# Kernel tuning notes

Hardware: AMD Instinct MI355X
Metric: run time of the kernel (lower is better)

## Reference

```python
import jax, jax.numpy as jnp
import numpy as np

E = 1024
H = 16
D = E // H
B = 32
S = 1024


def _layernorm(x, gamma, beta, eps=1e-5):
    mu = jnp.mean(x, axis=-1, keepdims=True)
    var = jnp.var(x, axis=-1, keepdims=True)
    return (x - mu) * jax.lax.rsqrt(var + eps) * gamma + beta


def setup_inputs() -> dict:
    key = jax.random.key(0)
    ks = jax.random.split(key, 16)
    w = lambda k, shape: jax.random.normal(k, shape, dtype=jnp.float32) * 0.02
    return {
        "img_feat": jax.random.normal(ks[0], (B, S, E), dtype=jnp.float32),
        "heat_feat": jax.random.normal(ks[1], (B, E), dtype=jnp.float32),
        "W_img": w(ks[2], (E, E)), "b_img": jnp.zeros((E,), jnp.float32),
        "W_heat": w(ks[3], (E, E)), "b_heat": jnp.zeros((E,), jnp.float32),
        "Wq": w(ks[4], (E, E)), "bq": jnp.zeros((E,), jnp.float32),
        "Wk": w(ks[5], (E, E)), "bk": jnp.zeros((E,), jnp.float32),
        "Wv": w(ks[6], (E, E)), "bv": jnp.zeros((E,), jnp.float32),
        "Wo": w(ks[7], (E, E)), "bo": jnp.zeros((E,), jnp.float32),
        "gamma": jnp.ones((E,), jnp.float32),
        "beta": jnp.zeros((E,), jnp.float32),
    }


def reference(img_feat, heat_feat, W_img, b_img, W_heat, b_heat,
              Wq, bq, Wk, bk, Wv, bv, Wo, bo, gamma, beta):
    # projections (torch Linear: x @ W.T + b)
    proj_heat = (heat_feat @ W_heat.T + b_heat)[:, None, :]        # [B,1,E]
    proj_img = img_feat @ W_img.T + b_img                          # [B,S,E]
    # multi-head attention, KV seq len = 1
    q = (proj_img @ Wq.T + bq).reshape(B, S, H, D)
    k = (proj_heat @ Wk.T + bk).reshape(B, 1, H, D)
    v = (proj_heat @ Wv.T + bv).reshape(B, 1, H, D)
    scale = 1.0 / np.sqrt(D).astype(np.float32)
    scores = jnp.einsum('bshd,bthd->bhst', q, k) * scale           # [B,H,S,1]
    attn = jax.nn.softmax(scores, axis=-1)                         # == ones
    ctx = jnp.einsum('bhst,bthd->bshd', attn, v).reshape(B, S, E)
    attn_out = ctx @ Wo.T + bo                                     # [B,S,E]
    # residual + LayerNorm (dropout is identity in eval)
    return _layernorm(img_feat + attn_out, gamma, beta)
```

## Files before the change

kernel.cpp:

```cpp
#include <hip/hip_runtime.h>


#define E_DIM 1024
#define B_DIM 32
#define S_DIM 1024

__global__ __launch_bounds__(256) void gemv_f32(
        const float* __restrict__ W,
        const float* __restrict__ bias,
        const float* __restrict__ x,
        float* __restrict__ y) {
    int wave = threadIdx.x >> 6;
    int lane = threadIdx.x & 63;
    int out_idx = (blockIdx.x << 2) + wave;
    int b = out_idx >> 10;
    int e = out_idx & (E_DIM - 1);
    const float4* w4 = reinterpret_cast<const float4*>(W + (size_t)e * E_DIM);
    const float4* x4 = reinterpret_cast<const float4*>(x + (size_t)b * E_DIM);
    float acc = 0.f;
    #pragma unroll
    for (int p = 0; p < 4; ++p) {
        float4 wv = w4[p * 64 + lane];
        float4 xv = x4[p * 64 + lane];
        acc += wv.x * xv.x + wv.y * xv.y + wv.z * xv.z + wv.w * xv.w;
    }
    #pragma unroll
    for (int off = 32; off; off >>= 1)
        acc += __shfl_down(acc, off, 64);
    if (lane == 0) y[out_idx] = acc + bias[e];
}

__global__ __launch_bounds__(256) void resid_layernorm(
        const float* __restrict__ img,
        const float* __restrict__ a,
        const float* __restrict__ gamma,
        const float* __restrict__ beta,
        float* __restrict__ out) {
    const int row = blockIdx.x;
    const int b = row >> 10;
    const int t = threadIdx.x;

    const float4* imgp = reinterpret_cast<const float4*>(img + (size_t)row * E_DIM);
    const float4* ap   = reinterpret_cast<const float4*>(a + (size_t)b * E_DIM);

    float4 iv = imgp[t];
    float4 av = ap[t];

    float x0 = iv.x + av.x;
    float x1 = iv.y + av.y;
    float x2 = iv.z + av.z;
    float x3 = iv.w + av.w;

    float s = x0 + x1 + x2 + x3;
    float q = x0 * x0 + x1 * x1 + x2 * x2 + x3 * x3;

    #pragma unroll
    for (int off = 32; off; off >>= 1) {
        s += __shfl_down(s, off, 64);
        q += __shfl_down(q, off, 64);
    }

    __shared__ float ssum[4], sqq[4];
    int wv = t >> 6, ln = t & 63;
    if (ln == 0) { ssum[wv] = s; sqq[wv] = q; }
    __syncthreads();
    if (t == 0) {
        float S = ssum[0] + ssum[1] + ssum[2] + ssum[3];
        float Q = sqq[0] + sqq[1] + sqq[2] + sqq[3];
        float mu = S * (1.0f / E_DIM);
        float var = Q * (1.0f / E_DIM) - mu * mu;
        ssum[0] = mu;
        sqq[0] = rsqrtf(var + 1e-5f);
    }
    __syncthreads();
    float mu = ssum[0];
    float rstd = sqq[0];

    const float4* gp = reinterpret_cast<const float4*>(gamma) + t;
    const float4* bp = reinterpret_cast<const float4*>(beta) + t;
    float4 gv = *gp, bv = *bp;

    float4 ov;
    ov.x = (x0 - mu) * rstd * gv.x + bv.x;
    ov.y = (x1 - mu) * rstd * gv.y + bv.y;
    ov.z = (x2 - mu) * rstd * gv.z + bv.z;
    ov.w = (x3 - mu) * rstd * gv.w + bv.w;

    reinterpret_cast<float4*>(out + (size_t)row * E_DIM)[t] = ov;
}

extern "C" void kernel_launch(void* const* d_in, const int* in_sizes, int n_in,
                              void* d_out, int out_size, void* d_ws, size_t ws_size,
                              hipStream_t stream) {
    const float* heat   = (const float*)d_in[1];
    const float* W_heat = (const float*)d_in[4];
    const float* b_heat = (const float*)d_in[5];
    const float* Wv     = (const float*)d_in[10];
    const float* bvv    = (const float*)d_in[11];
    const float* Wo     = (const float*)d_in[12];
    const float* bo     = (const float*)d_in[13];
    const float* img    = (const float*)d_in[0];
    const float* gamma  = (const float*)d_in[14];
    const float* beta   = (const float*)d_in[15];
    float* out = (float*)d_out;

    float* ws = (float*)d_ws;
    float* tt = ws;
    float* vv = ws + B_DIM * E_DIM;
    float* aa = ws + 2 * B_DIM * E_DIM;

    const int n_be = B_DIM * E_DIM;
    const int gemv_blocks = n_be / 4;

    gemv_f32<<<gemv_blocks, 256, 0, stream>>>(W_heat, b_heat, heat, tt);
    gemv_f32<<<gemv_blocks, 256, 0, stream>>>(Wv, bvv, tt, vv);
    gemv_f32<<<gemv_blocks, 256, 0, stream>>>(Wo, bo, vv, aa);

    resid_layernorm<<<B_DIM * S_DIM, 256, 0, stream>>>(img, aa, gamma, beta, out);
}
```

Before: 295.1 us.

## Reuse weight rows across 8 batches in GEMV and use wave-per-row layernorm

```diff
diff --git a/kernel.cpp b/kernel.cpp
--- a/kernel.cpp
+++ b/kernel.cpp
@@ -5,29 +5,40 @@
 #define B_DIM 32
 #define S_DIM 1024
 
-__global__ __launch_bounds__(256) void gemv_f32(
+__global__ __launch_bounds__(256) void gemv8_f32(
         const float* __restrict__ W,
         const float* __restrict__ bias,
         const float* __restrict__ x,
         float* __restrict__ y) {
-    int wave = threadIdx.x >> 6;
-    int lane = threadIdx.x & 63;
-    int out_idx = (blockIdx.x << 2) + wave;
-    int b = out_idx >> 10;
-    int e = out_idx & (E_DIM - 1);
+    const int w    = blockIdx.x * 4 + (threadIdx.x >> 6);
+    const int lane = threadIdx.x & 63;
+    const int e    = w >> 2;
+    const int b0   = (w & 3) * 8;
+
     const float4* w4 = reinterpret_cast<const float4*>(W + (size_t)e * E_DIM);
-    const float4* x4 = reinterpret_cast<const float4*>(x + (size_t)b * E_DIM);
-    float acc = 0.f;
+    float acc[8] = {0.f, 0.f, 0.f, 0.f, 0.f, 0.f, 0.f, 0.f};
+
     #pragma unroll
     for (int p = 0; p < 4; ++p) {
         float4 wv = w4[p * 64 + lane];
-        float4 xv = x4[p * 64 + lane];
-        acc += wv.x * xv.x + wv.y * xv.y + wv.z * xv.z + wv.w * xv.w;
+        #pragma unroll
+        for (int j = 0; j < 8; ++j) {
+            const float4* x4 =
+                reinterpret_cast<const float4*>(x + (size_t)(b0 + j) * E_DIM);
+            float4 xv = x4[p * 64 + lane];
+            acc[j] += wv.x * xv.x + wv.y * xv.y + wv.z * xv.z + wv.w * xv.w;
+        }
     }
+
+    const float be = bias[e];
     #pragma unroll
-    for (int off = 32; off; off >>= 1)
-        acc += __shfl_down(acc, off, 64);
-    if (lane == 0) y[out_idx] = acc + bias[e];
+    for (int j = 0; j < 8; ++j) {
+        float v = acc[j];
+        #pragma unroll
+        for (int off = 32; off; off >>= 1)
+            v += __shfl_down(v, off, 64);
+        if (lane == 0) y[(size_t)(b0 + j) * E_DIM + e] = v + be;
+    }
 }
 
 __global__ __launch_bounds__(256) void resid_layernorm(
@@ -36,62 +47,59 @@
         const float* __restrict__ gamma,
         const float* __restrict__ beta,
         float* __restrict__ out) {
-    const int row = blockIdx.x;
-    const int b = row >> 10;
-    const int t = threadIdx.x;
+    const int row  = blockIdx.x * 4 + (threadIdx.x >> 6);
+    const int lane = threadIdx.x & 63;
+    const int b    = row >> 10;
 
-    const float4* imgp = reinterpret_cast<const float4*>(img + (size_t)row * E_DIM);
-    const float4* ap   = reinterpret_cast<const float4*>(a + (size_t)b * E_DIM);
+    const float4* ip = reinterpret_cast<const float4*>(img + (size_t)row * E_DIM);
+    const float4* ap = reinterpret_cast<const float4*>(a + (size_t)b * E_DIM);
 
-    float4 iv = imgp[t];
-    float4 av = ap[t];
-
-    float x0 = iv.x + av.x;
-    float x1 = iv.y + av.y;
-    float x2 = iv.z + av.z;
-    float x3 = iv.w + av.w;
-
-    float s = x0 + x1 + x2 + x3;
-    float q = x0 * x0 + x1 * x1 + x2 * x2 + x3 * x3;
+    float4 xv[4];
+    float s = 0.f, q = 0.f;
+    #pragma unroll
+    for (int p = 0; p < 4; ++p) {
+        float4 iv = ip[p * 64 + lane];
+        float4 av = ap[p * 64 + lane];
+        float4 x;
+        x.x = iv.x + av.x;
+        x.y = iv.y + av.y;
+        x.z = iv.z + av.z;
+        x.w = iv.w + av.w;
+        xv[p] = x;
+        s += x.x + x.y + x.z + x.w;
+        q += x.x * x.x + x.y * x.y + x.z * x.z + x.w * x.w;
+    }
 
     #pragma unroll
     for (int off = 32; off; off >>= 1) {
-        s += __shfl_down(s, off, 64);
-        q += __shfl_down(q, off, 64);
+        s += __shfl_xor(s, off, 64);
+        q += __shfl_xor(q, off, 64);
     }
 
-    __shared__ float ssum[4], sqq[4];
-    int wv = t >> 6, ln = t & 63;
-    if (ln == 0) { ssum[wv] = s; sqq[wv] = q; }
-    __syncthreads();
-    if (t == 0) {
-        float S = ssum[0] + ssum[1] + ssum[2] + ssum[3];
-        float Q = sqq[0] + sqq[1] + sqq[2] + sqq[3];
-        float mu = S * (1.0f / E_DIM);
-        float var = Q * (1.0f / E_DIM) - mu * mu;
-        ssum[0] = mu;
-        sqq[0] = rsqrtf(var + 1e-5f);
+    const float mu   = s * (1.0f / E_DIM);
+    const float rstd = rsqrtf(q * (1.0f / E_DIM) - mu * mu + 1e-5f);
+
+    const float4* gp = reinterpret_cast<const float4*>(gamma);
+    const float4* bp = reinterpret_cast<const float4*>(beta);
+    float4* op = reinterpret_cast<float4*>(out + (size_t)row * E_DIM);
+
+    #pragma unroll
+    for (int p = 0; p < 4; ++p) {
+        float4 g  = gp[p * 64 + lane];
+        float4 be = bp[p * 64 + lane];
+        float4 o;
+        o.x = (xv[p].x - mu) * rstd * g.x + be.x;
+        o.y = (xv[p].y - mu) * rstd * g.y + be.y;
+        o.z = (xv[p].z - mu) * rstd * g.z + be.z;
+        o.w = (xv[p].w - mu) * rstd * g.w + be.w;
+        op[p * 64 + lane] = o;
     }
-    __syncthreads();
-    float mu = ssum[0];
-    float rstd = sqq[0];
-
-    const float4* gp = reinterpret_cast<const float4*>(gamma) + t;
-    const float4* bp = reinterpret_cast<const float4*>(beta) + t;
-    float4 gv = *gp, bv = *bp;
-
-    float4 ov;
-    ov.x = (x0 - mu) * rstd * gv.x + bv.x;
-    ov.y = (x1 - mu) * rstd * gv.y + bv.y;
-    ov.z = (x2 - mu) * rstd * gv.z + bv.z;
-    ov.w = (x3 - mu) * rstd * gv.w + bv.w;
-
-    reinterpret_cast<float4*>(out + (size_t)row * E_DIM)[t] = ov;
 }
 
 extern "C" void kernel_launch(void* const* d_in, const int* in_sizes, int n_in,
                               void* d_out, int out_size, void* d_ws, size_t ws_size,
                               hipStream_t stream) {
+    const float* img    = (const float*)d_in[0];
     const float* heat   = (const float*)d_in[1];
     const float* W_heat = (const float*)d_in[4];
     const float* b_heat = (const float*)d_in[5];
@@ -99,7 +107,6 @@
     const float* bvv    = (const float*)d_in[11];
     const float* Wo     = (const float*)d_in[12];
     const float* bo     = (const float*)d_in[13];
-    const float* img    = (const float*)d_in[0];
     const float* gamma  = (const float*)d_in[14];
     const float* beta   = (const float*)d_in[15];
     float* out = (float*)d_out;
@@ -109,12 +116,9 @@
     float* vv = ws + B_DIM * E_DIM;
     float* aa = ws + 2 * B_DIM * E_DIM;
 
-    const int n_be = B_DIM * E_DIM;
-    const int gemv_blocks = n_be / 4;
+    gemv8_f32<<<1024, 256, 0, stream>>>(W_heat, b_heat, heat, tt);
+    gemv8_f32<<<1024, 256, 0, stream>>>(Wv, bvv, tt, vv);
+    gemv8_f32<<<1024, 256, 0, stream>>>(Wo, bo, vv, aa);
 
-    gemv_f32<<<gemv_blocks, 256, 0, stream>>>(W_heat, b_heat, heat, tt);
-    gemv_f32<<<gemv_blocks, 256, 0, stream>>>(Wv, bvv, tt, vv);
-    gemv_f32<<<gemv_blocks, 256, 0, stream>>>(Wo, bo, vv, aa);
-
-    resid_layernorm<<<B_DIM * S_DIM, 256, 0, stream>>>(img, aa, gamma, beta, out);
+    resid_layernorm<<<8192, 256, 0, stream>>>(img, aa, gamma, beta, out);
 }
```

After: 295.1 us. No clear change (+0.0%).
